# Kernel optimization log

Hardware: AMD Instinct MI355X
Metric: run time of the kernel (lower is better)

The kernel has to match this reference:

```python
import jax, jax.numpy as jnp
import numpy as np

B, L, D, HD = 4, 4096, 2048, 128

def setup_inputs() -> dict:
    key = jax.random.key(0)
    ks = jax.random.split(key, 9)
    s = 0.02  # keep logits in a sane range
    return {
        "x": jax.random.normal(ks[0], (B, L, D), jnp.float32),
        "Wq": jax.random.normal(ks[1], (D, HD), jnp.float32) * s,
        "bq": jax.random.normal(ks[2], (HD,), jnp.float32) * s,
        "Wk": jax.random.normal(ks[3], (D, HD), jnp.float32) * s,
        "bk": jax.random.normal(ks[4], (HD,), jnp.float32) * s,
        "Wv": jax.random.normal(ks[5], (D, HD), jnp.float32) * s,
        "bv": jax.random.normal(ks[6], (HD,), jnp.float32) * s,
        "Wo": jax.random.normal(ks[7], (HD, D), jnp.float32) * s,
        "bo": jax.random.normal(ks[8], (D,), jnp.float32) * s,
    }

def reference(x, Wq, bq, Wk, bk, Wv, bv, Wo, bo):
    # x: (B, L, D)
    q = x @ Wq + bq                      # (B, L, HD)
    k = x @ Wk + bk
    v = x @ Wv + bv
    hd = q.shape[-1]
    scores = jnp.einsum('bqd,bkd->bqk', q, k) / jnp.sqrt(jnp.float32(hd))
    Lq = x.shape[1]
    causal = jnp.tril(jnp.ones((Lq, Lq), dtype=bool))  # (L, L)
    scores = jnp.where(causal, scores, -jnp.inf)
    weights = jax.nn.softmax(scores, axis=-1)          # (B, L, L)
    out = jnp.einsum('bqk,bkd->bqd', weights, v)       # (B, L, HD)
    return out @ Wo + bo                               # (B, L, D)
```

## Files before the change

kernel.cpp:

```cpp
#include <hip/hip_runtime.h>

#define B_  4
#define L_  4096
#define D_  2048
#define HD_ 128
#define M_  (B_*L_)

typedef __attribute__((ext_vector_type(8))) short short8;
typedef __attribute__((ext_vector_type(4))) float f32x4;
typedef __attribute__((ext_vector_type(16))) float f32x16;
typedef __attribute__((ext_vector_type(4))) unsigned short u16x4;
typedef __attribute__((ext_vector_type(4))) unsigned int u32x4;
typedef unsigned short u16;

__device__ __forceinline__ u16 f2bf(float f){
  union { float f; unsigned u; } v; v.f = f;
  unsigned r = v.u + 0x7FFFu + ((v.u >> 16) & 1u);
  return (u16)(r >> 16);
}

__device__ __forceinline__ unsigned cvtpk_bf16(float a, float b){
  unsigned r;
  asm volatile("v_cvt_pk_bf16_f32 %0, %1, %2" : "=v"(r) : "v"(a), "v"(b));
  return r;
}

__global__ __launch_bounds__(256) void prepw_kernel(
    const float* __restrict__ Wq, const float* __restrict__ Wk,
    const float* __restrict__ Wv, const float* __restrict__ Wo,
    u16* __restrict__ Wf_qkv, u16* __restrict__ Wf_o)
{
  __shared__ float T[64][68];
  const int tid = threadIdx.x;
  int tb = blockIdx.x;
  int mat = tb >> 6, tt = tb & 63;
  const float* src; int Cw, rt, ct;
  if (mat < 3) {
    src = (mat==0) ? Wq : (mat==1) ? Wk : Wv;
    Cw = HD_; rt = tt >> 1; ct = tt & 1;
  } else {
    src = Wo;
    Cw = D_; rt = tt >> 5; ct = tt & 31;
  }
  int r0 = rt*64, c0 = ct*64;
  #pragma unroll
  for (int i=0;i<4;i++){
    int fid = i*256 + tid;
    int row = fid >> 4, c4 = (fid & 15) * 4;
    float4 v = *reinterpret_cast<const float4*>(src + (size_t)(r0+row)*Cw + c0 + c4);
    *reinterpret_cast<float4*>(&T[row][c4]) = v;
  }
  __syncthreads();
  #pragma unroll
  for (int i=0;i<2;i++){
    int sid = i*256 + tid;
    int crow = sid >> 3, k8 = (sid & 7) * 8;
    short8 o;
    #pragma unroll
    for (int j=0;j<8;j++) o[j] = (short)f2bf(T[k8+j][crow]);
    int K = r0 + k8;
    if (mat < 3) {
      int C = mat*128 + c0 + crow;
      size_t off = ((size_t)(K>>4)*12 + (C>>5))*512
                 + ((((K>>3)&1))*32 + (C&31))*8;
      *reinterpret_cast<short8*>(Wf_qkv + off) = o;
    } else {
      int C = c0 + crow;
      size_t off = ((size_t)(K>>5)*128 + (C>>4))*512
                 + ((((K>>3)&3))*16 + (C&15))*8;
      *reinterpret_cast<short8*>(Wf_o + off) = o;
    }
  }
}

__global__ __launch_bounds__(256) void prepx_kernel(
    const float* __restrict__ x, u16* __restrict__ xbf)
{
  int cid  = blockIdx.x*4 + (threadIdx.x >> 6);
  int lane = threadIdx.x & 63;
  int l31 = lane & 31, hi = lane >> 5;
  int rs = cid >> 7, t = cid & 127;
  const float* src = x + (size_t)(rs*32 + l31)*D_ + t*16 + hi*8;
  float4 f0 = *reinterpret_cast<const float4*>(src);
  float4 f1 = *reinterpret_cast<const float4*>(src + 4);
  union { u32x4 u; short8 s8; } o;
  o.u[0] = cvtpk_bf16(f0.x, f0.y);
  o.u[1] = cvtpk_bf16(f0.z, f0.w);
  o.u[2] = cvtpk_bf16(f1.x, f1.y);
  o.u[3] = cvtpk_bf16(f1.z, f1.w);
  *reinterpret_cast<short8*>(xbf + (size_t)cid*512 + lane*8) = o.s8;
}

__global__ __launch_bounds__(256, 2) void qkv_kernel(
    const u16* __restrict__ xbf, const u16* __restrict__ Wf,
    const float* __restrict__ bq, const float* __restrict__ bk,
    const float* __restrict__ bv,
    u16* __restrict__ Q, u16* __restrict__ Kf, u16* __restrict__ Vf)
{
  const int rb = blockIdx.x;
  const int tid = threadIdx.x;
  const int lane = tid & 63, wc = tid >> 6;
  const int l31 = lane & 31, hi = lane >> 5;

  const u16* aP = xbf + ((size_t)rb*128)*512 + lane*8;
  const u16* bP = Wf  + (size_t)(wc*3)*512 + lane*8;

  f32x16 acc[3];
  #pragma unroll
  for (int nb=0;nb<3;nb++)
    #pragma unroll
    for (int i=0;i<16;i++) acc[nb][i] = 0.f;

  short8 gaA[4], gbA[4][3], gaB[4], gbB[4][3];

  #pragma unroll
  for (int s=0;s<4;s++){
    gaA[s] = *reinterpret_cast<const short8*>(aP + (size_t)s*512);
    #pragma unroll
    for (int n=0;n<3;n++)
      gbA[s][n] = *reinterpret_cast<const short8*>(bP + ((size_t)s*12 + n)*512);
  }

  #pragma unroll 1
  for (int g = 0; g < 32; g += 2) {
    if (g + 1 < 32) {
      const u16* ap = aP + (size_t)(g+1)*4*512;
      const u16* bp = bP + (size_t)(g+1)*48*512;
      #pragma unroll
      for (int s=0;s<4;s++){
        gaB[s] = *reinterpret_cast<const short8*>(ap + (size_t)s*512);
        #pragma unroll
        for (int n=0;n<3;n++)
          gbB[s][n] = *reinterpret_cast<const short8*>(bp + ((size_t)s*12 + n)*512);
      }
    }
    __builtin_amdgcn_s_setprio(1);
    #pragma unroll
    for (int s=0;s<4;s++)
      #pragma unroll
      for (int n=0;n<3;n++)
        acc[n] = __builtin_amdgcn_mfma_f32_32x32x16_bf16(gaA[s], gbA[s][n], acc[n], 0, 0, 0);
    __builtin_amdgcn_s_setprio(0);
    if (g + 2 < 32) {
      const u16* ap = aP + (size_t)(g+2)*4*512;
      const u16* bp = bP + (size_t)(g+2)*48*512;
      #pragma unroll
      for (int s=0;s<4;s++){
        gaA[s] = *reinterpret_cast<const short8*>(ap + (size_t)s*512);
        #pragma unroll
        for (int n=0;n<3;n++)
          gbA[s][n] = *reinterpret_cast<const short8*>(bp + ((size_t)s*12 + n)*512);
      }
    }
    __builtin_amdgcn_s_setprio(1);
    #pragma unroll
    for (int s=0;s<4;s++)
      #pragma unroll
      for (int n=0;n<3;n++)
        acc[n] = __builtin_amdgcn_mfma_f32_32x32x16_bf16(gaB[s], gbB[s][n], acc[n], 0, 0, 0);
    __builtin_amdgcn_s_setprio(0);
  }

  const float qscale = 0.08838834764831845f;
  const int bb = rb >> 7;
  const int kt = (rb & 127) >> 1;
  const int n2 = rb & 1;
  const size_t kvBase = ((size_t)bb*64 + kt)*16;
  #pragma unroll
  for (int nb=0; nb<3; nb++){
    const int colbase = wc*96 + nb*32;
    const int j = colbase >> 7;
    const int col = colbase + l31;
    const int c = col & 127;
    const float bi = (j==0) ? bq[c] : (j==1) ? bk[c] : bv[c];
    if (j == 0) {
      #pragma unroll
      for (int r=0;r<16;r++){
        int row = rb*32 + 4*hi + (r&3) + 8*(r>>2);
        Q[(size_t)row*HD_ + c] = f2bf((acc[nb][r] + bi) * qscale);
      }
    } else if (j == 1) {
      int ksd = c >> 4, hid = (c >> 3) & 1, jd = c & 7;
      #pragma unroll
      for (int r=0;r<16;r++){
        int l31k = 8*(r>>2) + 4*hi + (r&3);
        Kf[(kvBase + n2*8 + ksd)*512 + (hid*32 + l31k)*8 + jd]
            = f2bf(acc[nb][r] + bi);
      }
    } else {
      int nbv = c >> 5;
      #pragma unroll
      for (int g2=0; g2<4; g2++){
        int ksv = n2*2 + (g2>>1), hiv = g2&1, j0 = 4*hi;
        u16x4 v4;
        #pragma unroll
        for (int q=0;q<4;q++) v4[q] = f2bf(acc[nb][4*g2+q] + bi);
        *reinterpret_cast<u16x4*>(
            Vf + (kvBase + ksv*4 + nbv)*512 + (hiv*32 + l31)*8 + j0) = v4;
      }
    }
  }
}

__global__ __launch_bounds__(256, 2) void attn_kernel(
    const u16* __restrict__ Qg, const u16* __restrict__ Kfg,
    const u16* __restrict__ Vfg, u16* __restrict__ AOf)
{
  const int blk = blockIdx.x;
  const int xcd = blk & 7;
  const int sub = blk >> 3;
  const int b   = xcd >> 1;
  const int strip = 127 - (2*sub + (xcd & 1));
  const int q0  = strip * 32;
  const int KT  = (strip >> 1) + 1;

  const int tid = threadIdx.x, lane = tid & 63, w = tid >> 6;
  const int l31 = lane & 31;
  const int hi  = lane >> 5;

  const u16* Qb  = Qg  + (size_t)b * L_ * HD_;
  const u16* Kfb = Kfg + (size_t)b * 64 * 8192 + lane*8;
  const u16* Vfb = Vfg + (size_t)b * 64 * 8192 + lane*8;

  __shared__ __attribute__((aligned(16))) float Ol[4][32][132];
  __shared__ float Ml[4][32], Ll[4][32];

  short8 qf[8];
  #pragma unroll
  for (int ks=0; ks<8; ks++)
    qf[ks] = *reinterpret_cast<const short8*>(
        &Qb[(size_t)(q0 + l31)*HD_ + ks*16 + hi*8]);

  f32x16 O[4];
  #pragma unroll
  for (int nb=0; nb<4; nb++)
    #pragma unroll
    for (int i=0;i<16;i++) O[nb][i] = 0.f;
  float m_ = -__builtin_inff();
  float l_ = 0.f;

  for (int kt = w; kt < KT; kt += 4) {
    const u16* Kt = Kfb + (size_t)kt*8192;
    f32x16 s[2];
    #pragma unroll
    for (int n=0;n<2;n++)
      #pragma unroll
      for (int i=0;i<16;i++) s[n][i] = 0.f;
    __builtin_amdgcn_s_setprio(1);
    #pragma unroll
    for (int ks=0;ks<8;ks++)
      #pragma unroll
      for (int n=0;n<2;n++){
        short8 ka = *reinterpret_cast<const short8*>(Kt + (n*8 + ks)*512);
        s[n] = __builtin_amdgcn_mfma_f32_32x32x16_bf16(ka, qf[ks], s[n], 0, 0, 0);
      }
    __builtin_amdgcn_s_setprio(0);

    if (kt == KT-1) {
      #pragma unroll
      for (int n=0;n<2;n++)
        #pragma unroll
        for (int reg=0;reg<16;reg++){
          int key = kt*64 + n*32 + (reg&3) + 8*(reg>>2) + 4*hi;
          if (key > q0 + l31) s[n][reg] = -__builtin_inff();
        }
    }

    float pmax = s[0][0];
    #pragma unroll
    for (int n=0;n<2;n++)
      #pragma unroll
      for (int reg=0;reg<16;reg++) pmax = fmaxf(pmax, s[n][reg]);
    pmax = fmaxf(pmax, __shfl_xor(pmax, 32, 64));

    if (!__all(pmax <= m_ + 8.f)) {
      float mnew = fmaxf(m_, pmax);
      float alpha = __expf(m_ - mnew);
      m_ = mnew;
      l_ *= alpha;
      #pragma unroll
      for (int nb=0; nb<4; nb++)
        #pragma unroll
        for (int i=0;i<16;i++) O[nb][i] *= alpha;
    }

    float rsum = 0.f;
    #pragma unroll
    for (int n=0;n<2;n++)
      #pragma unroll
      for (int reg=0;reg<16;reg++){
        float p = __expf(s[n][reg] - m_);
        s[n][reg] = p;
        rsum += p;
      }
    rsum += __shfl_xor(rsum, 32, 64);
    l_ += rsum;

    unsigned c[2][8], ox[2][8];
    #pragma unroll
    for (int n=0;n<2;n++)
      #pragma unroll
      for (int i=0;i<8;i++)
        c[n][i] = cvtpk_bf16(s[n][2*i], s[n][2*i+1]);
    #pragma unroll
    for (int n=0;n<2;n++)
      #pragma unroll
      for (int i=0;i<8;i++)
        ox[n][i] = (unsigned)__shfl_xor((int)c[n][i], 32, 64);

    short8 pb[4];
    #pragma unroll
    for (int n=0;n<2;n++)
      #pragma unroll
      for (int sB=0;sB<2;sB++){
        union { u32x4 u; short8 s8; } t;
        t.u[0] = hi ? ox[n][4*sB+2] : c[n][4*sB+0];
        t.u[1] = hi ? ox[n][4*sB+3] : c[n][4*sB+1];
        t.u[2] = hi ? c[n][4*sB+2]  : ox[n][4*sB+0];
        t.u[3] = hi ? c[n][4*sB+3]  : ox[n][4*sB+1];
        pb[2*n+sB] = t.s8;
      }

    const u16* Vt2 = Vfb + (size_t)kt*8192;
    __builtin_amdgcn_s_setprio(1);
    #pragma unroll
    for (int ks=0; ks<4; ks++){
      #pragma unroll
      for (int nb=0; nb<4; nb++){
        short8 av = *reinterpret_cast<const short8*>(Vt2 + (ks*4 + nb)*512);
        O[nb] = __builtin_amdgcn_mfma_f32_32x32x16_bf16(av, pb[ks], O[nb], 0, 0, 0);
      }
    }
    __builtin_amdgcn_s_setprio(0);
  }

  if (hi == 0) { Ml[w][l31] = m_; Ll[w][l31] = l_; }
  #pragma unroll
  for (int nb=0; nb<4; nb++)
    #pragma unroll
    for (int g=0; g<4; g++){
      f32x4 v;
      v[0]=O[nb][4*g+0]; v[1]=O[nb][4*g+1]; v[2]=O[nb][4*g+2]; v[3]=O[nb][4*g+3];
      *reinterpret_cast<f32x4*>(&Ol[w][l31][nb*32 + g*8 + hi*4]) = v;
    }
  __syncthreads();

  {
    int q  = tid >> 3;
    int dc = (tid & 7) * 16;
    float mw[4], lw[4];
    float M = -__builtin_inff();
    #pragma unroll
    for (int w2=0; w2<4; w2++){ mw[w2]=Ml[w2][q]; lw[w2]=Ll[w2][q]; M = fmaxf(M, mw[w2]); }
    float den = 0.f, cw[4];
    #pragma unroll
    for (int w2=0; w2<4; w2++){ float e = __expf(mw[w2]-M); cw[w2]=e; den += lw[w2]*e; }
    float inv = 1.0f/den;
    float o[16];
    #pragma unroll
    for (int j=0;j<16;j++) o[j] = 0.f;
    #pragma unroll
    for (int w2=0; w2<4; w2++){
      #pragma unroll
      for (int g=0; g<4; g++){
        f32x4 p = *reinterpret_cast<const f32x4*>(&Ol[w2][q][dc + g*4]);
        #pragma unroll
        for (int j=0;j<4;j++) o[g*4+j] += cw[w2]*p[j];
      }
    }
    short8 st0, st1;
    #pragma unroll
    for (int j=0;j<8;j++){ st0[j] = (short)f2bf(o[j]*inv); st1[j] = (short)f2bf(o[8+j]*inv); }
    size_t rowg = (size_t)b*L_ + q0 + q;
    size_t rb2g = rowg >> 5;
    int qq = (int)(rowg & 31);
    int mA = qq >> 4, l15A = qq & 15;
    int ks0 = dc >> 5,      lh0 = (dc >> 3) & 3;
    int ks1 = (dc+8) >> 5,  lh1 = ((dc+8) >> 3) & 3;
    *reinterpret_cast<short8*>(AOf + ((rb2g*4 + ks0)*2 + mA)*512 + (lh0*16 + l15A)*8) = st0;
    *reinterpret_cast<short8*>(AOf + ((rb2g*4 + ks1)*2 + mA)*512 + (lh1*16 + l15A)*8) = st1;
  }
}

__global__ __launch_bounds__(256) void proj_kernel(
    const u16* __restrict__ AOf, const u16* __restrict__ Wf_o,
    const float* __restrict__ bo, float* __restrict__ out)
{
  const int nb  = blockIdx.x;
  const int rbk = blockIdx.y;
  const int tid = threadIdx.x, lane = tid & 63, w = tid >> 6;
  const int l15 = lane & 15, lhi = lane >> 4;

  const u16* faBase = AOf  + (size_t)rbk*8*512 + lane*8;
  const u16* fbBase = Wf_o + lane*8;

  f32x4 acc[2][4];
  f32x4 zero4 = {0.f,0.f,0.f,0.f};
  #pragma unroll
  for (int m=0;m<2;m++)
    #pragma unroll
    for (int n=0;n<4;n++) acc[m][n] = zero4;

  #pragma unroll
  for (int ks=0; ks<4; ks++){
    short8 fa[2], fb[4];
    #pragma unroll
    for (int m=0;m<2;m++)
      fa[m] = *reinterpret_cast<const short8*>(faBase + (ks*2 + m)*512);
    #pragma unroll
    for (int n=0;n<4;n++)
      fb[n] = *reinterpret_cast<const short8*>(
          fbBase + (size_t)(ks*128 + nb*16 + w*4 + n)*512);
    #pragma unroll
    for (int m=0;m<2;m++)
      #pragma unroll
      for (int n=0;n<4;n++)
        acc[m][n] = __builtin_amdgcn_mfma_f32_16x16x32_bf16(fa[m], fb[n], acc[m][n], 0, 0, 0);
  }

  #pragma unroll
  for (int n=0;n<4;n++){
    int col = nb*256 + w*64 + n*16 + l15;
    float bi = bo[col];
    #pragma unroll
    for (int m=0;m<2;m++){
      int row = rbk*32 + m*16 + (lhi<<2);
      #pragma unroll
      for (int r=0;r<4;r++)
        out[(size_t)(row+r)*D_ + col] = acc[m][n][r] + bi;
    }
  }
}

extern "C" void kernel_launch(void* const* d_in, const int* in_sizes, int n_in,
                              void* d_out, int out_size, void* d_ws, size_t ws_size,
                              hipStream_t stream) {
  const float* x  = (const float*)d_in[0];
  const float* Wq = (const float*)d_in[1];
  const float* bq = (const float*)d_in[2];
  const float* Wk = (const float*)d_in[3];
  const float* bk = (const float*)d_in[4];
  const float* Wv = (const float*)d_in[5];
  const float* bv = (const float*)d_in[6];
  const float* Wo = (const float*)d_in[7];
  const float* bo = (const float*)d_in[8];
  float* out = (float*)d_out;

  u16* ws      = (u16*)d_ws;
  u16* Wf_qkv  = ws;
  u16* Wf_o    = Wf_qkv + 3*HD_*D_;
  u16* Q       = Wf_o   + (size_t)D_*HD_;
  u16* Kf      = Q + (size_t)M_*HD_;
  u16* Vf      = Kf + (size_t)M_*HD_;
  u16* AOf     = Vf + (size_t)M_*HD_;
  u16* xbf     = AOf + (size_t)M_*HD_;

  prepw_kernel<<<256, 256, 0, stream>>>(Wq, Wk, Wv, Wo, Wf_qkv, Wf_o);
  prepx_kernel<<<16384, 256, 0, stream>>>(x, xbf);
  qkv_kernel<<<512, 256, 0, stream>>>(xbf, Wf_qkv, bq, bk, bv, Q, Kf, Vf);
  attn_kernel<<<512, 256, 0, stream>>>(Q, Kf, Vf, AOf);
  proj_kernel<<<dim3(8, 512), 256, 0, stream>>>(AOf, Wf_o, bo, out);
}
```

Before: 191.2 us.

## Fuse fp32-to-bf16 x conversion into QKV GEMM and use 64-row blocks

Drops the separate prepx kernel that converted x to bf16 into a fragment layout. The QKV GEMM now loads fp32 x rows directly with float4 loads and packs them to bf16 in registers before each MFMA. Blocks grow to 512 threads covering 64 rows, so two row-waves share the same weight fragments. This removes a full write and re-read of the bf16 copy of x and one launch, but doubles the A-operand bytes loaded inside the GEMM and adds conversion instructions to the hot loop.

```diff
diff --git a/kernel.cpp b/kernel.cpp
--- a/kernel.cpp
+++ b/kernel.cpp
@@ -73,37 +73,20 @@
   }
 }
 
-__global__ __launch_bounds__(256) void prepx_kernel(
-    const float* __restrict__ x, u16* __restrict__ xbf)
-{
-  int cid  = blockIdx.x*4 + (threadIdx.x >> 6);
-  int lane = threadIdx.x & 63;
-  int l31 = lane & 31, hi = lane >> 5;
-  int rs = cid >> 7, t = cid & 127;
-  const float* src = x + (size_t)(rs*32 + l31)*D_ + t*16 + hi*8;
-  float4 f0 = *reinterpret_cast<const float4*>(src);
-  float4 f1 = *reinterpret_cast<const float4*>(src + 4);
-  union { u32x4 u; short8 s8; } o;
-  o.u[0] = cvtpk_bf16(f0.x, f0.y);
-  o.u[1] = cvtpk_bf16(f0.z, f0.w);
-  o.u[2] = cvtpk_bf16(f1.x, f1.y);
-  o.u[3] = cvtpk_bf16(f1.z, f1.w);
-  *reinterpret_cast<short8*>(xbf + (size_t)cid*512 + lane*8) = o.s8;
-}
-
-__global__ __launch_bounds__(256, 2) void qkv_kernel(
-    const u16* __restrict__ xbf, const u16* __restrict__ Wf,
+__global__ __launch_bounds__(512, 2) void qkv_kernel(
+    const float* __restrict__ x, const u16* __restrict__ Wf,
     const float* __restrict__ bq, const float* __restrict__ bk,
     const float* __restrict__ bv,
     u16* __restrict__ Q, u16* __restrict__ Kf, u16* __restrict__ Vf)
 {
   const int rb = blockIdx.x;
   const int tid = threadIdx.x;
-  const int lane = tid & 63, wc = tid >> 6;
+  const int lane = tid & 63, w = tid >> 6;
+  const int wr = w >> 2, wc = w & 3;
   const int l31 = lane & 31, hi = lane >> 5;
 
-  const u16* aP = xbf + ((size_t)rb*128)*512 + lane*8;
-  const u16* bP = Wf  + (size_t)(wc*3)*512 + lane*8;
+  const float* aP = x + (size_t)(rb*64 + wr*32 + l31)*D_ + hi*8;
+  const u16*   bP = Wf + (size_t)(wc*3)*512 + lane*8;
 
   f32x16 acc[3];
   #pragma unroll
@@ -111,11 +94,13 @@
     #pragma unroll
     for (int i=0;i<16;i++) acc[nb][i] = 0.f;
 
-  short8 gaA[4], gbA[4][3], gaB[4], gbB[4][3];
+  float4 a0A[4], a1A[4], a0B[4], a1B[4];
+  short8 gbA[4][3], gbB[4][3];
 
   #pragma unroll
   for (int s=0;s<4;s++){
-    gaA[s] = *reinterpret_cast<const short8*>(aP + (size_t)s*512);
+    a0A[s] = *reinterpret_cast<const float4*>(aP + (size_t)s*16);
+    a1A[s] = *reinterpret_cast<const float4*>(aP + (size_t)s*16 + 4);
     #pragma unroll
     for (int n=0;n<3;n++)
       gbA[s][n] = *reinterpret_cast<const short8*>(bP + ((size_t)s*12 + n)*512);
@@ -124,11 +109,12 @@
   #pragma unroll 1
   for (int g = 0; g < 32; g += 2) {
     if (g + 1 < 32) {
-      const u16* ap = aP + (size_t)(g+1)*4*512;
-      const u16* bp = bP + (size_t)(g+1)*48*512;
+      const float* ap = aP + (size_t)(g+1)*4*16;
+      const u16*   bp = bP + (size_t)(g+1)*48*512;
       #pragma unroll
       for (int s=0;s<4;s++){
-        gaB[s] = *reinterpret_cast<const short8*>(ap + (size_t)s*512);
+        a0B[s] = *reinterpret_cast<const float4*>(ap + (size_t)s*16);
+        a1B[s] = *reinterpret_cast<const float4*>(ap + (size_t)s*16 + 4);
         #pragma unroll
         for (int n=0;n<3;n++)
           gbB[s][n] = *reinterpret_cast<const short8*>(bp + ((size_t)s*12 + n)*512);
@@ -136,17 +122,24 @@
     }
     __builtin_amdgcn_s_setprio(1);
     #pragma unroll
-    for (int s=0;s<4;s++)
+    for (int s=0;s<4;s++){
+      union { u32x4 u; short8 s8; } fa;
+      fa.u[0] = cvtpk_bf16(a0A[s].x, a0A[s].y);
+      fa.u[1] = cvtpk_bf16(a0A[s].z, a0A[s].w);
+      fa.u[2] = cvtpk_bf16(a1A[s].x, a1A[s].y);
+      fa.u[3] = cvtpk_bf16(a1A[s].z, a1A[s].w);
       #pragma unroll
       for (int n=0;n<3;n++)
-        acc[n] = __builtin_amdgcn_mfma_f32_32x32x16_bf16(gaA[s], gbA[s][n], acc[n], 0, 0, 0);
+        acc[n] = __builtin_amdgcn_mfma_f32_32x32x16_bf16(fa.s8, gbA[s][n], acc[n], 0, 0, 0);
+    }
     __builtin_amdgcn_s_setprio(0);
     if (g + 2 < 32) {
-      const u16* ap = aP + (size_t)(g+2)*4*512;
-      const u16* bp = bP + (size_t)(g+2)*48*512;
+      const float* ap = aP + (size_t)(g+2)*4*16;
+      const u16*   bp = bP + (size_t)(g+2)*48*512;
       #pragma unroll
       for (int s=0;s<4;s++){
-        gaA[s] = *reinterpret_cast<const short8*>(ap + (size_t)s*512);
+        a0A[s] = *reinterpret_cast<const float4*>(ap + (size_t)s*16);
+        a1A[s] = *reinterpret_cast<const float4*>(ap + (size_t)s*16 + 4);
         #pragma unroll
         for (int n=0;n<3;n++)
           gbA[s][n] = *reinterpret_cast<const short8*>(bp + ((size_t)s*12 + n)*512);
@@ -154,17 +147,22 @@
     }
     __builtin_amdgcn_s_setprio(1);
     #pragma unroll
-    for (int s=0;s<4;s++)
+    for (int s=0;s<4;s++){
+      union { u32x4 u; short8 s8; } fa;
+      fa.u[0] = cvtpk_bf16(a0B[s].x, a0B[s].y);
+      fa.u[1] = cvtpk_bf16(a0B[s].z, a0B[s].w);
+      fa.u[2] = cvtpk_bf16(a1B[s].x, a1B[s].y);
+      fa.u[3] = cvtpk_bf16(a1B[s].z, a1B[s].w);
       #pragma unroll
       for (int n=0;n<3;n++)
-        acc[n] = __builtin_amdgcn_mfma_f32_32x32x16_bf16(gaB[s], gbB[s][n], acc[n], 0, 0, 0);
+        acc[n] = __builtin_amdgcn_mfma_f32_32x32x16_bf16(fa.s8, gbB[s][n], acc[n], 0, 0, 0);
+    }
     __builtin_amdgcn_s_setprio(0);
   }
 
   const float qscale = 0.08838834764831845f;
-  const int bb = rb >> 7;
-  const int kt = (rb & 127) >> 1;
-  const int n2 = rb & 1;
+  const int bb = rb >> 6;
+  const int kt = rb & 63;
   const size_t kvBase = ((size_t)bb*64 + kt)*16;
   #pragma unroll
   for (int nb=0; nb<3; nb++){
@@ -176,7 +174,7 @@
     if (j == 0) {
       #pragma unroll
       for (int r=0;r<16;r++){
-        int row = rb*32 + 4*hi + (r&3) + 8*(r>>2);
+        int row = rb*64 + wr*32 + 4*hi + (r&3) + 8*(r>>2);
         Q[(size_t)row*HD_ + c] = f2bf((acc[nb][r] + bi) * qscale);
       }
     } else if (j == 1) {
@@ -184,14 +182,14 @@
       #pragma unroll
       for (int r=0;r<16;r++){
         int l31k = 8*(r>>2) + 4*hi + (r&3);
-        Kf[(kvBase + n2*8 + ksd)*512 + (hid*32 + l31k)*8 + jd]
+        Kf[(kvBase + wr*8 + ksd)*512 + (hid*32 + l31k)*8 + jd]
             = f2bf(acc[nb][r] + bi);
       }
     } else {
       int nbv = c >> 5;
       #pragma unroll
       for (int g2=0; g2<4; g2++){
-        int ksv = n2*2 + (g2>>1), hiv = g2&1, j0 = 4*hi;
+        int ksv = wr*2 + (g2>>1), hiv = g2&1, j0 = 4*hi;
         u16x4 v4;
         #pragma unroll
         for (int q=0;q<4;q++) v4[q] = f2bf(acc[nb][4*g2+q] + bi);
@@ -453,11 +451,9 @@
   u16* Kf      = Q + (size_t)M_*HD_;
   u16* Vf      = Kf + (size_t)M_*HD_;
   u16* AOf     = Vf + (size_t)M_*HD_;
-  u16* xbf     = AOf + (size_t)M_*HD_;
 
   prepw_kernel<<<256, 256, 0, stream>>>(Wq, Wk, Wv, Wo, Wf_qkv, Wf_o);
-  prepx_kernel<<<16384, 256, 0, stream>>>(x, xbf);
-  qkv_kernel<<<512, 256, 0, stream>>>(xbf, Wf_qkv, bq, bk, bv, Q, Kf, Vf);
+  qkv_kernel<<<256, 512, 0, stream>>>(x, Wf_qkv, bq, bk, bv, Q, Kf, Vf);
   attn_kernel<<<512, 256, 0, stream>>>(Q, Kf, Vf, AOf);
   proj_kernel<<<dim3(8, 512), 256, 0, stream>>>(AOf, Wf_o, bo, out);
 }
```

Result: slower. 208.4 us (+9.0%).
